# Optimization experiments

Measured on AMD Instinct MI355X. Metric: run time of the kernel, lower is better.

The kernel has to match this reference:

```python
import jax, jax.numpy as jnp
import numpy as np

N_REVIEWS = 500000
N_ITEMS = 100000
N_USERS = 200000
D = 128           # per-entity embedding dim
INPUT_DIM = 3 * D # 384
OUTPUT_DIM = 128


def setup_inputs() -> dict:
    key = jax.random.key(0)
    k1, k2, k3, k4, k5, k6 = jax.random.split(key, 6)
    review_embedding = jax.random.normal(k1, (N_REVIEWS, D), dtype=jnp.float32)
    item_embedding = jax.random.normal(k2, (N_ITEMS, D), dtype=jnp.float32)
    user_embedding = jax.random.normal(k3, (N_USERS, D), dtype=jnp.float32)
    adj_user_idx = jax.random.randint(k4, (N_REVIEWS,), 0, N_USERS, dtype=jnp.int32)
    adj_item_idx = jax.random.randint(k5, (N_REVIEWS,), 0, N_ITEMS, dtype=jnp.int32)
    agg_weights = jax.random.normal(k6, (INPUT_DIM, OUTPUT_DIM), dtype=jnp.float32) * 0.05
    return {
        "review_embedding": review_embedding,
        "item_embedding": item_embedding,
        "user_embedding": user_embedding,
        "adj_user_idx": adj_user_idx,
        "adj_item_idx": adj_item_idx,
        "agg_weights": agg_weights,
    }


def reference(review_embedding, item_embedding, user_embedding,
              adj_user_idx, adj_item_idx, agg_weights):
    # Gather neighbor embeddings (tf.nn.embedding_lookup)
    review_item = item_embedding[adj_item_idx]  # [N_reviews, D]
    review_user = user_embedding[adj_user_idx]  # [N_reviews, D]
    # Concat along feature axis -> [N_reviews, 3D], then dense + activation
    agg_vector = jnp.concatenate([review_embedding, review_user, review_item], axis=1)
    return jax.nn.relu(agg_vector @ agg_weights)
```

## Files before the change

### kernel.cpp

```cpp
#include <hip/hip_runtime.h>
#include <hip/hip_bf16.h>

#define NREV 500000
#define DIM  128
#define KDIM 384

typedef __attribute__((ext_vector_type(4))) float f32x4;
typedef __attribute__((ext_vector_type(8))) short bf16x8;

__device__ __forceinline__ unsigned short f2bf_s(float x) {
    unsigned int u = __builtin_bit_cast(unsigned int, x);
    u = (u + 0x7FFFu + ((u >> 16) & 1u)) >> 16;
    return (unsigned short)u;
}

__global__ void wconv_kernel(const float* __restrict__ W,
                             unsigned short* __restrict__ Bw) {
    int e = blockIdx.x * 256 + threadIdx.x;
    if (e < 12 * 8 * 64 * 8) {
        int j  = e & 7;
        int l  = (e >> 3) & 63;
        int fg = (e >> 9) & 7;
        int ks = e >> 12;
        int n = fg * 16 + (l & 15);
        int k = ks * 32 + ((l >> 4) << 3) + j;
        Bw[e] = f2bf_s(W[k * DIM + n]);
    }
}

__device__ __forceinline__ void gload_lds16(const void* g, void* l) {
    __builtin_amdgcn_global_load_lds(
        (const __attribute__((address_space(1))) void*)g,
        (__attribute__((address_space(3))) void*)l, 16, 0, 0);
}

__device__ __forceinline__ unsigned int pk2(float lo, float hi) {
    return __builtin_amdgcn_perm(__builtin_bit_cast(unsigned int, hi),
                                 __builtin_bit_cast(unsigned int, lo),
                                 0x07060302u);
}
__device__ __forceinline__ bf16x8 cvt8(f32x4 a, f32x4 b) {
    union { bf16x8 v; unsigned int u[4]; } U;
    U.u[0] = pk2(a[0], a[1]);
    U.u[1] = pk2(a[2], a[3]);
    U.u[2] = pk2(b[0], b[1]);
    U.u[3] = pk2(b[2], b[3]);
    return U.v;
}

__global__ __launch_bounds__(256, 3) void agg_kernel(
    const float* __restrict__ rev,
    const float* __restrict__ item,
    const float* __restrict__ user,
    const int*   __restrict__ uidx,
    const int*   __restrict__ iidx,
    const unsigned short* __restrict__ Bw,
    float* __restrict__ out)
{
    __shared__ __align__(16) float Atile[3][128 * 32];

    const int r0   = blockIdx.x * 128;
    const int t    = threadIdx.x;
    const int wid  = t >> 6, lane = t & 63;
    const int wr   = wid >> 1, wc = wid & 1;
    const int lm   = lane & 15, lk = lane >> 4;

    const int srow = t >> 3;
    const int cswz = ((t & 7) ^ ((t >> 3) & 7)) << 2;

    const float* pr[4]; const float* pu[4]; const float* pi[4];
    #pragma unroll
    for (int it = 0; it < 4; ++it) {
        int gr = r0 + it * 32 + srow;
        if (gr >= NREV) gr = NREV - 1;
        pr[it] = rev  + (size_t)gr * DIM + cswz;
        pu[it] = user + (size_t)uidx[gr] * DIM + cswz;
        pi[it] = item + (size_t)iidx[gr] * DIM + cswz;
    }

    f32x4 acc[4][4];
    #pragma unroll
    for (int i = 0; i < 4; ++i)
        #pragma unroll
        for (int j = 0; j < 4; ++j)
            acc[i][j] = (f32x4){0.f, 0.f, 0.f, 0.f};

    const int axor  = (lm & 7) << 4;
    const int koff0 = (lk * 32) ^ axor;
    const unsigned short* bbase = Bw + ((wc * 4) * 64 + lane) * 8;

    auto prefetchA = [&](int s, int buf) {
        const int cb = (s & 3) * 32;
        #pragma unroll
        for (int it = 0; it < 4; ++it) {
            const float* src = ((s < 4) ? pr[it] : (s < 8) ? pu[it] : pi[it]) + cb;
            gload_lds16(src, (char*)&Atile[buf][0] + it * 4096 + t * 16);
        }
    };
    bf16x8 breg[3][4];
    auto loadB = [&](int s, bf16x8* dst) {
        #pragma unroll
        for (int nf = 0; nf < 4; ++nf)
            dst[nf] = *reinterpret_cast<const bf16x8*>(
                bbase + (size_t)(s * 8 + nf) * 512);
    };

    auto step = [&](int s) {
        const char* la = (const char*)&Atile[s % 3][0];
        const bf16x8* bf = breg[s % 3];
        #pragma unroll
        for (int mf = 0; mf < 4; ++mf) {
            int rb = (wr * 64 + mf * 16 + lm) * 128;
            f32x4 f0 = *reinterpret_cast<const f32x4*>(la + rb + koff0);
            f32x4 f1 = *reinterpret_cast<const f32x4*>(la + rb + (koff0 ^ 16));
            bf16x8 af = cvt8(f0, f1);
            #pragma unroll
            for (int nf = 0; nf < 4; ++nf)
                acc[mf][nf] = __builtin_amdgcn_mfma_f32_16x16x32_bf16(
                    af, bf[nf], acc[mf][nf], 0, 0, 0);
        }
    };

    prefetchA(0, 0); loadB(0, breg[0]);
    prefetchA(1, 1); loadB(1, breg[1]);

    #pragma unroll
    for (int s = 0; s < 12; ++s) {
        if (s == 11) { asm volatile("s_waitcnt vmcnt(0)" ::: "memory"); }
        else         { asm volatile("s_waitcnt vmcnt(8)" ::: "memory"); }
        __builtin_amdgcn_s_barrier();
        asm volatile("" ::: "memory");
        if (s < 10) {
            prefetchA(s + 2, (s + 2) % 3);
            loadB(s + 2, breg[(s + 2) % 3]);
        }
        step(s);
    }

    #pragma unroll
    for (int mf = 0; mf < 4; ++mf) {
        #pragma unroll
        for (int j = 0; j < 4; ++j) {
            int row = r0 + wr * 64 + mf * 16 + lk * 4 + j;
            if (row < NREV) {
                float* orow = out + (size_t)row * DIM + wc * 64;
                #pragma unroll
                for (int nf = 0; nf < 4; ++nf)
                    orow[nf * 16 + lm] = fmaxf(acc[mf][nf][j], 0.0f);
            }
        }
    }
}

extern "C" void kernel_launch(void* const* d_in, const int* in_sizes, int n_in,
                              void* d_out, int out_size, void* d_ws, size_t ws_size,
                              hipStream_t stream) {
    const float* rev  = (const float*)d_in[0];
    const float* item = (const float*)d_in[1];
    const float* user = (const float*)d_in[2];
    const int*   uidx = (const int*)d_in[3];
    const int*   iidx = (const int*)d_in[4];
    const float* W    = (const float*)d_in[5];
    unsigned short* Bw = (unsigned short*)d_ws;
    float* out = (float*)d_out;

    wconv_kernel<<<192, 256, 0, stream>>>(W, Bw);

    int nblocks = (NREV + 127) / 128;
    agg_kernel<<<nblocks, 256, 0, stream>>>(rev, item, user, uidx, iidx, Bw, out);
}
```

Measured before the change: 182.4 us.

## Precompute projected user/item tables and gather bf16 projections in epilogue

Splits the weight matrix into review, user and item blocks. A new pre-pass multiplies every user and item table row by its weight block and stores the results as bf16. The main kernel then runs a K=128 GEMM over review embeddings only, and in the epilogue gathers and adds the precomputed user and item projections before the ReLU. This cuts GEMM work to a third and halves the bytes per gathered row. In exchange it adds an extra kernel pass over 300k table rows, exposes unpipelined gather latency in the epilogue, and adds bf16 rounding error on the projections.

```diff
diff --git a/kernel.cpp b/kernel.cpp
--- a/kernel.cpp
+++ b/kernel.cpp
@@ -1,30 +1,45 @@
 #include <hip/hip_runtime.h>
 #include <hip/hip_bf16.h>
 
-#define NREV 500000
-#define DIM  128
-#define KDIM 384
+#define NREV  500000
+#define NUSER 200000
+#define NITEM 100000
+#define DIM   128
+
+#define WR_OFF 0
+#define WU_OFF 16384
+#define WI_OFF 32768
+#define U2_OFF 49152
+#define I2_OFF (49152 + NUSER * 128)
+#define UBLK 1563
+#define IBLK 782
 
 typedef __attribute__((ext_vector_type(4))) float f32x4;
 typedef __attribute__((ext_vector_type(8))) short bf16x8;
+typedef __attribute__((ext_vector_type(4))) unsigned short u16x4;
 
 __device__ __forceinline__ unsigned short f2bf_s(float x) {
     unsigned int u = __builtin_bit_cast(unsigned int, x);
     u = (u + 0x7FFFu + ((u >> 16) & 1u)) >> 16;
     return (unsigned short)u;
 }
+__device__ __forceinline__ float bf2f(unsigned short u) {
+    return __builtin_bit_cast(float, (unsigned int)u << 16);
+}
 
 __global__ void wconv_kernel(const float* __restrict__ W,
-                             unsigned short* __restrict__ Bw) {
+                             unsigned short* __restrict__ ws) {
     int e = blockIdx.x * 256 + threadIdx.x;
-    if (e < 12 * 8 * 64 * 8) {
-        int j  = e & 7;
-        int l  = (e >> 3) & 63;
-        int fg = (e >> 9) & 7;
-        int ks = e >> 12;
+    if (e < 3 * 16384) {
+        int e14 = e & 16383;
+        int b  = e >> 14;
+        int ks = e14 >> 12;
+        int fg = (e14 >> 9) & 7;
+        int l  = (e14 >> 3) & 63;
+        int j  = e14 & 7;
         int n = fg * 16 + (l & 15);
-        int k = ks * 32 + ((l >> 4) << 3) + j;
-        Bw[e] = f2bf_s(W[k * DIM + n]);
+        int k = b * 128 + ks * 32 + ((l >> 4) << 3) + j;
+        ws[e] = f2bf_s(W[k * DIM + n]);
     }
 }
 
@@ -48,18 +63,20 @@
     return U.v;
 }
 
-__global__ __launch_bounds__(256, 3) void agg_kernel(
-    const float* __restrict__ rev,
+__global__ __launch_bounds__(256, 3) void precomp_kernel(
+    const float* __restrict__ user,
     const float* __restrict__ item,
-    const float* __restrict__ user,
-    const int*   __restrict__ uidx,
-    const int*   __restrict__ iidx,
-    const unsigned short* __restrict__ Bw,
-    float* __restrict__ out)
+    unsigned short* __restrict__ ws)
 {
     __shared__ __align__(16) float Atile[3][128 * 32];
 
-    const int r0   = blockIdx.x * 128;
+    const bool isU = blockIdx.x < UBLK;
+    const float* tab = isU ? user : item;
+    const int M      = isU ? NUSER : NITEM;
+    const unsigned short* wf = ws + (isU ? WU_OFF : WI_OFF);
+    unsigned short* P2       = ws + (isU ? U2_OFF : I2_OFF);
+    const int r0 = (isU ? blockIdx.x : blockIdx.x - UBLK) * 128;
+
     const int t    = threadIdx.x;
     const int wid  = t >> 6, lane = t & 63;
     const int wr   = wid >> 1, wc = wid & 1;
@@ -68,14 +85,12 @@
     const int srow = t >> 3;
     const int cswz = ((t & 7) ^ ((t >> 3) & 7)) << 2;
 
-    const float* pr[4]; const float* pu[4]; const float* pi[4];
+    const float* pr[4];
     #pragma unroll
     for (int it = 0; it < 4; ++it) {
         int gr = r0 + it * 32 + srow;
-        if (gr >= NREV) gr = NREV - 1;
-        pr[it] = rev  + (size_t)gr * DIM + cswz;
-        pu[it] = user + (size_t)uidx[gr] * DIM + cswz;
-        pi[it] = item + (size_t)iidx[gr] * DIM + cswz;
+        if (gr >= M) gr = M - 1;
+        pr[it] = tab + (size_t)gr * DIM + cswz;
     }
 
     f32x4 acc[4][4];
@@ -87,24 +102,20 @@
 
     const int axor  = (lm & 7) << 4;
     const int koff0 = (lk * 32) ^ axor;
-    const unsigned short* bbase = Bw + ((wc * 4) * 64 + lane) * 8;
+    const unsigned short* bbase = wf + ((wc * 4) * 64 + lane) * 8;
 
     auto prefetchA = [&](int s, int buf) {
-        const int cb = (s & 3) * 32;
-        #pragma unroll
-        for (int it = 0; it < 4; ++it) {
-            const float* src = ((s < 4) ? pr[it] : (s < 8) ? pu[it] : pi[it]) + cb;
-            gload_lds16(src, (char*)&Atile[buf][0] + it * 4096 + t * 16);
-        }
+        const int cb = s * 32;
+        #pragma unroll
+        for (int it = 0; it < 4; ++it)
+            gload_lds16(pr[it] + cb, (char*)&Atile[buf][0] + it * 4096 + t * 16);
     };
     bf16x8 breg[3][4];
     auto loadB = [&](int s, bf16x8* dst) {
         #pragma unroll
         for (int nf = 0; nf < 4; ++nf)
-            dst[nf] = *reinterpret_cast<const bf16x8*>(
-                bbase + (size_t)(s * 8 + nf) * 512);
-    };
-
+            dst[nf] = *reinterpret_cast<const bf16x8*>(bbase + (size_t)(s * 8 + nf) * 512);
+    };
     auto step = [&](int s) {
         const char* la = (const char*)&Atile[s % 3][0];
         const bf16x8* bf = breg[s % 3];
@@ -125,15 +136,108 @@
     prefetchA(1, 1); loadB(1, breg[1]);
 
     #pragma unroll
-    for (int s = 0; s < 12; ++s) {
-        if (s == 11) { asm volatile("s_waitcnt vmcnt(0)" ::: "memory"); }
-        else         { asm volatile("s_waitcnt vmcnt(8)" ::: "memory"); }
+    for (int s = 0; s < 4; ++s) {
+        if (s == 3) { asm volatile("s_waitcnt vmcnt(0)" ::: "memory"); }
+        else        { asm volatile("s_waitcnt vmcnt(8)" ::: "memory"); }
         __builtin_amdgcn_s_barrier();
         asm volatile("" ::: "memory");
-        if (s < 10) {
-            prefetchA(s + 2, (s + 2) % 3);
-            loadB(s + 2, breg[(s + 2) % 3]);
-        }
+        if (s < 2) { prefetchA(s + 2, (s + 2) % 3); loadB(s + 2, breg[(s + 2) % 3]); }
+        step(s);
+    }
+
+    #pragma unroll
+    for (int mf = 0; mf < 4; ++mf) {
+        #pragma unroll
+        for (int j = 0; j < 4; ++j) {
+            int row = r0 + wr * 64 + mf * 16 + lk * 4 + j;
+            if (row < M) {
+                u16x4 v;
+                #pragma unroll
+                for (int nf = 0; nf < 4; ++nf)
+                    v[nf] = f2bf_s(acc[mf][nf][j]);
+                *reinterpret_cast<u16x4*>(P2 + (size_t)row * 128 + wc * 64 + lm * 4) = v;
+            }
+        }
+    }
+}
+
+__global__ __launch_bounds__(256, 3) void agg_kernel(
+    const float* __restrict__ rev,
+    const int*   __restrict__ uidx,
+    const int*   __restrict__ iidx,
+    const unsigned short* __restrict__ ws,
+    float* __restrict__ out)
+{
+    __shared__ __align__(16) float Atile[3][128 * 32];
+
+    const int r0   = blockIdx.x * 128;
+    const int t    = threadIdx.x;
+    const int wid  = t >> 6, lane = t & 63;
+    const int wr   = wid >> 1, wc = wid & 1;
+    const int lm   = lane & 15, lk = lane >> 4;
+
+    const int srow = t >> 3;
+    const int cswz = ((t & 7) ^ ((t >> 3) & 7)) << 2;
+
+    const float* pr[4];
+    #pragma unroll
+    for (int it = 0; it < 4; ++it) {
+        int gr = r0 + it * 32 + srow;
+        if (gr >= NREV) gr = NREV - 1;
+        pr[it] = rev + (size_t)gr * DIM + cswz;
+    }
+
+    f32x4 acc[4][4];
+    #pragma unroll
+    for (int i = 0; i < 4; ++i)
+        #pragma unroll
+        for (int j = 0; j < 4; ++j)
+            acc[i][j] = (f32x4){0.f, 0.f, 0.f, 0.f};
+
+    const int axor  = (lm & 7) << 4;
+    const int koff0 = (lk * 32) ^ axor;
+    const unsigned short* bbase = ws + WR_OFF + ((wc * 4) * 64 + lane) * 8;
+    const unsigned short* U2 = ws + U2_OFF;
+    const unsigned short* I2 = ws + I2_OFF;
+
+    auto prefetchA = [&](int s, int buf) {
+        const int cb = s * 32;
+        #pragma unroll
+        for (int it = 0; it < 4; ++it)
+            gload_lds16(pr[it] + cb, (char*)&Atile[buf][0] + it * 4096 + t * 16);
+    };
+    bf16x8 breg[3][4];
+    auto loadB = [&](int s, bf16x8* dst) {
+        #pragma unroll
+        for (int nf = 0; nf < 4; ++nf)
+            dst[nf] = *reinterpret_cast<const bf16x8*>(bbase + (size_t)(s * 8 + nf) * 512);
+    };
+    auto step = [&](int s) {
+        const char* la = (const char*)&Atile[s % 3][0];
+        const bf16x8* bf = breg[s % 3];
+        #pragma unroll
+        for (int mf = 0; mf < 4; ++mf) {
+            int rb = (wr * 64 + mf * 16 + lm) * 128;
+            f32x4 f0 = *reinterpret_cast<const f32x4*>(la + rb + koff0);
+            f32x4 f1 = *reinterpret_cast<const f32x4*>(la + rb + (koff0 ^ 16));
+            bf16x8 af = cvt8(f0, f1);
+            #pragma unroll
+            for (int nf = 0; nf < 4; ++nf)
+                acc[mf][nf] = __builtin_amdgcn_mfma_f32_16x16x32_bf16(
+                    af, bf[nf], acc[mf][nf], 0, 0, 0);
+        }
+    };
+
+    prefetchA(0, 0); loadB(0, breg[0]);
+    prefetchA(1, 1); loadB(1, breg[1]);
+
+    #pragma unroll
+    for (int s = 0; s < 4; ++s) {
+        if (s == 3) { asm volatile("s_waitcnt vmcnt(0)" ::: "memory"); }
+        else        { asm volatile("s_waitcnt vmcnt(8)" ::: "memory"); }
+        __builtin_amdgcn_s_barrier();
+        asm volatile("" ::: "memory");
+        if (s < 2) { prefetchA(s + 2, (s + 2) % 3); loadB(s + 2, breg[(s + 2) % 3]); }
         step(s);
     }
 
@@ -143,10 +247,16 @@
         for (int j = 0; j < 4; ++j) {
             int row = r0 + wr * 64 + mf * 16 + lk * 4 + j;
             if (row < NREV) {
+                int u = uidx[row], i = iidx[row];
+                u16x4 gu = *reinterpret_cast<const u16x4*>(
+                    U2 + (size_t)u * 128 + wc * 64 + lm * 4);
+                u16x4 gi = *reinterpret_cast<const u16x4*>(
+                    I2 + (size_t)i * 128 + wc * 64 + lm * 4);
                 float* orow = out + (size_t)row * DIM + wc * 64;
                 #pragma unroll
                 for (int nf = 0; nf < 4; ++nf)
-                    orow[nf * 16 + lm] = fmaxf(acc[mf][nf][j], 0.0f);
+                    orow[nf * 16 + lm] =
+                        fmaxf(acc[mf][nf][j] + bf2f(gu[nf]) + bf2f(gi[nf]), 0.0f);
             }
         }
     }
@@ -161,11 +271,12 @@
     const int*   uidx = (const int*)d_in[3];
     const int*   iidx = (const int*)d_in[4];
     const float* W    = (const float*)d_in[5];
-    unsigned short* Bw = (unsigned short*)d_ws;
+    unsigned short* ws = (unsigned short*)d_ws;
     float* out = (float*)d_out;
 
-    wconv_kernel<<<192, 256, 0, stream>>>(W, Bw);
+    wconv_kernel<<<192, 256, 0, stream>>>(W, ws);
+    precomp_kernel<<<UBLK + IBLK, 256, 0, stream>>>(user, item, ws);
 
     int nblocks = (NREV + 127) / 128;
-    agg_kernel<<<nblocks, 256, 0, stream>>>(rev, item, user, uidx, iidx, Bw, out);
-}
+    agg_kernel<<<nblocks, 256, 0, stream>>>(rev, uidx, iidx, ws, out);
+}
```

After: 221.1 us. +21.2%, slower.
